# Kernel tuning notes

Measured on AMD Instinct MI355X. Metric: run time of the kernel, lower is better.

Reference implementation:

```python
import jax, jax.numpy as jnp
import numpy as np

B, N, EPG = 64, 512, 8192
E = B * EPG
K1 = int(np.ceil(0.8 * N))    # 410
K2 = int(np.ceil(0.8 * K1))   # 328


def setup_inputs() -> dict:
    key = jax.random.key(0)
    ks = jax.random.split(key, 32)
    x = jax.random.normal(ks[0], (B * N, 32), jnp.float32)
    edge_attr = jax.random.normal(ks[1], (E, 100), jnp.float32)
    src_l = jax.random.randint(ks[2], (E,), 0, N)
    dst_l = jax.random.randint(ks[3], (E,), 0, N)
    off = jnp.repeat(jnp.arange(B, dtype=jnp.int64) * N, EPG)
    edge_index = jnp.stack([src_l + off, dst_l + off]).astype(jnp.int64)
    batch = jnp.repeat(jnp.arange(B, dtype=jnp.int64), N)

    def lin(k, fin, fout):
        s = 1.0 / np.sqrt(fin)
        k1, k2 = jax.random.split(k)
        return (jax.random.uniform(k1, (fin, fout), jnp.float32, -s, s),
                jax.random.uniform(k2, (fout,), jnp.float32, -s, s))

    dec1_w, dec1_b = lin(ks[4], 100, 64)
    dec2_w, dec2_b = lin(ks[5], 64, 32)
    mlp1_w, mlp1_b = lin(ks[6], 32, 128)
    mlp2_w, mlp2_b = lin(ks[7], 128, 256)
    pool1_w = jax.random.normal(ks[8], (256,), jnp.float32) * 0.1
    gat_w = jax.random.normal(ks[9], (256, 256), jnp.float32) * (1.0 / np.sqrt(256))
    gat_att_src = jax.random.normal(ks[10], (4, 64), jnp.float32) * 0.1
    gat_att_dst = jax.random.normal(ks[11], (4, 64), jnp.float32) * 0.1
    gat_b = jnp.zeros((256,), jnp.float32)
    pool2_w = jax.random.normal(ks[12], (256,), jnp.float32) * 0.1
    lin1_w, lin1_b = lin(ks[13], 512, 128)
    lin2_w, lin2_b = lin(ks[14], 128, 64)
    lin3_w, lin3_b = lin(ks[15], 64, 2)
    return dict(x=x, edge_index=edge_index, batch=batch, edge_attr=edge_attr,
                dec1_w=dec1_w, dec1_b=dec1_b, dec2_w=dec2_w, dec2_b=dec2_b,
                mlp1_w=mlp1_w, mlp1_b=mlp1_b, mlp2_w=mlp2_w, mlp2_b=mlp2_b,
                pool1_w=pool1_w, gat_w=gat_w, gat_att_src=gat_att_src,
                gat_att_dst=gat_att_dst, gat_b=gat_b, pool2_w=pool2_w,
                lin1_w=lin1_w, lin1_b=lin1_b, lin2_w=lin2_w, lin2_b=lin2_b,
                lin3_w=lin3_w, lin3_b=lin3_b)


def _forward(x, edge_attr, dec1_w, dec1_b, dec2_w, dec2_b, mlp1_w, mlp1_b,
             mlp2_w, mlp2_b, pool1_w, gat_w, gat_att_src, gat_att_dst, gat_b,
             pool2_w, lin1_w, lin1_b, lin2_w, lin2_b, lin3_w, lin3_b,
             src, dst):
    # edge encoder
    ea = jax.nn.relu(edge_attr @ dec1_w + dec1_b)
    ea = jax.nn.relu(ea @ dec2_w + dec2_b)                       # [E,32]
    # GINEConv (eps=0): sum_j relu(x_j + e_ji), then mlp((1+eps)x + aggr)
    msg = jax.nn.relu(x[src] + ea)
    agg = jax.ops.segment_sum(msg, dst, num_segments=B * N)
    h = x + agg
    h = jax.nn.relu(h @ mlp1_w + mlp1_b) @ mlp2_w + mlp2_b       # [BN,256]
    h = jax.nn.relu(h)
    # TopKPooling 1 (uniform graphs -> fixed k)
    s = jnp.tanh((h @ pool1_w) / jnp.linalg.norm(pool1_w))       # [BN]
    topv, topi = jax.lax.top_k(s.reshape(B, N), K1)              # [B,K1]
    gperm = (topi + jnp.arange(B)[:, None] * N).reshape(-1)
    hp = h[gperm] * topv.reshape(-1)[:, None]                    # [B*K1,256]
    kept = jnp.zeros(B * N, bool).at[gperm].set(True)
    newid = jnp.zeros(B * N, jnp.int32).at[gperm].set(jnp.arange(B * K1, dtype=jnp.int32))
    src1, dst1 = newid[src], newid[dst]
    valid = kept[src] & kept[dst]
    # readout 1: global max + mean pool
    hr = hp.reshape(B, K1, 256)
    x1 = jnp.concatenate([hr.max(axis=1), hr.mean(axis=1)], axis=-1)  # [B,512]
    # GATConv(256, 64, heads=4) with self-loops; invalid edges masked
    Nk = B * K1
    loops = jnp.arange(Nk, dtype=jnp.int32)
    src2 = jnp.concatenate([src1, loops])
    dst2 = jnp.concatenate([dst1, loops])
    valid2 = jnp.concatenate([valid, jnp.ones(Nk, bool)])
    xl = (hp @ gat_w).reshape(Nk, 4, 64)
    a_src = (xl * gat_att_src).sum(-1)                           # [Nk,4]
    a_dst = (xl * gat_att_dst).sum(-1)
    logit = jax.nn.leaky_relu(a_src[src2] + a_dst[dst2], 0.2)    # [E2,4]
    logit = jnp.where(valid2[:, None], logit, -jnp.inf)
    m = jax.ops.segment_max(logit, dst2, num_segments=Nk)
    e = jnp.where(valid2[:, None], jnp.exp(logit - m[dst2]), 0.0)
    den = jax.ops.segment_sum(e, dst2, num_segments=Nk)
    alpha = e / den[dst2]
    out = jax.ops.segment_sum(alpha[:, :, None] * xl[src2], dst2, num_segments=Nk)
    g = jax.nn.relu(out.reshape(Nk, 256) + gat_b)
    # TopKPooling 2 (pooled edges unused downstream)
    s2 = jnp.tanh((g @ pool2_w) / jnp.linalg.norm(pool2_w))
    topv2, topi2 = jax.lax.top_k(s2.reshape(B, K1), K2)
    gperm2 = (topi2 + jnp.arange(B)[:, None] * K1).reshape(-1)
    gp = (g[gperm2] * topv2.reshape(-1)[:, None]).reshape(B, K2, 256)
    x2 = jnp.concatenate([gp.max(axis=1), gp.mean(axis=1)], axis=-1)
    # head (dropout = identity in eval)
    z = x1 + x2
    z = jax.nn.relu(z @ lin1_w + lin1_b)
    z = jax.nn.relu(z @ lin2_w + lin2_b)
    return jax.nn.log_softmax(z @ lin3_w + lin3_b, axis=-1)     # [B,2]


def reference(x, edge_index, batch, edge_attr, dec1_w, dec1_b, dec2_w, dec2_b,
              mlp1_w, mlp1_b, mlp2_w, mlp2_b, pool1_w, gat_w, gat_att_src,
              gat_att_dst, gat_b, pool2_w, lin1_w, lin1_b, lin2_w, lin2_b,
              lin3_w, lin3_b):
    src = edge_index[0].astype(jnp.int32)
    dst = edge_index[1].astype(jnp.int32)
    return _forward(x, edge_attr, dec1_w, dec1_b, dec2_w, dec2_b, mlp1_w,
                    mlp1_b, mlp2_w, mlp2_b, pool1_w, gat_w, gat_att_src,
                    gat_att_dst, gat_b, pool2_w, lin1_w, lin1_b, lin2_w,
                    lin2_b, lin3_w, lin3_b, src, dst)
```

## Files before the change

### kernel.cpp

```cpp
#include <hip/hip_runtime.h>
#include <math.h>

#define B_   64
#define N_   512
#define E_   524288
#define BN_  32768
#define K1_  410
#define K2_  328
#define NK_  26240
#define KC_  25

__device__ __forceinline__ float lrelu(float x) { return x > 0.f ? x : 0.2f * x; }

__global__ __launch_bounds__(256) void norm_kernel(const float* __restrict__ p1,
                                                   const float* __restrict__ p2,
                                                   float* __restrict__ norms) {
    __shared__ float r1[256], r2[256];
    int t = threadIdx.x;
    float a = p1[t], b = p2[t];
    r1[t] = a * a; r2[t] = b * b;
    for (int o = 128; o > 0; o >>= 1) {
        __syncthreads();
        if (t < o) { r1[t] += r1[t + o]; r2[t] += r2[t + o]; }
    }
    __syncthreads();
    if (t == 0) { norms[0] = sqrtf(r1[0]); norms[1] = sqrtf(r2[0]); }
}

template <int NSEG>
__global__ __launch_bounds__(1024) void scan_kernel(int* __restrict__ cnt, int* __restrict__ offsets)
{
    __shared__ int part[1024];
    int t = threadIdx.x;
    const int CH = (NSEG + 1023) / 1024;
    int base = t * CH;
    int sum = 0;
    for (int i = 0; i < CH; ++i) { int gi = base + i; if (gi < NSEG) sum += cnt[gi]; }
    part[t] = sum;
    __syncthreads();
    for (int o = 1; o < 1024; o <<= 1) {
        int v = (t >= o) ? part[t - o] : 0;
        __syncthreads();
        part[t] += v;
        __syncthreads();
    }
    int run = (t == 0) ? 0 : part[t - 1];
    for (int i = 0; i < CH; ++i) {
        int gi = base + i;
        if (gi < NSEG) { offsets[gi] = run; run += cnt[gi]; cnt[gi] = 0; }
    }
    if (t == 1023) offsets[NSEG] = part[1023];
}

__global__ __launch_bounds__(256) void count_node_kernel(const int* __restrict__ dstG,
                                                         int* __restrict__ cnt_node)
{
    int e = blockIdx.x * blockDim.x + threadIdx.x;
    atomicAdd(&cnt_node[dstG[e]], 1);
}

__global__ __launch_bounds__(256) void fill_node_kernel(const int* __restrict__ dstG,
                                                        const int* __restrict__ offs_node,
                                                        int* __restrict__ cnt_node,
                                                        int* __restrict__ pos_e)
{
    int e = blockIdx.x * blockDim.x + threadIdx.x;
    int d = dstG[e];
    int p = offs_node[d] + atomicAdd(&cnt_node[d], 1);
    pos_e[e] = p;
}

__global__ __launch_bounds__(256) void edge_mlp_kernel(
    const float* __restrict__ edge_attr, const int* __restrict__ srcG,
    const int* __restrict__ pos_e,
    const float* __restrict__ x,
    const float* __restrict__ W1, const float* __restrict__ b1,
    const float* __restrict__ W2, const float* __restrict__ b2,
    float* __restrict__ msg_sorted)
{
    __shared__ float bufAT[KC_][68];
    __shared__ float w1cT[KC_][64];
    __shared__ float ea1T[64][68];
    __shared__ float w2s[64][32];
    __shared__ float b2s[32];
    __shared__ int   srcs[64], poss[64];

    int tid = threadIdx.x;
    int eb  = blockIdx.x * 64;

    if (tid < 64) { srcs[tid] = srcG[eb + tid]; poss[tid] = pos_e[eb + tid]; }
    for (int i = tid; i < 64 * 32; i += 256) w2s[i >> 5][i & 31] = W2[i];
    if (tid >= 192 && tid < 224) b2s[tid - 192] = b2[tid - 192];

    int tx = tid & 15, ty = tid >> 4;
    float b1v[4];
#pragma unroll
    for (int j = 0; j < 4; ++j) b1v[j] = b1[tx * 4 + j];

    int attr_base[7], lds_a[7];
    bool valid[7];
#pragma unroll
    for (int u = 0; u < 7; ++u) {
        int i = tid + u * 256;
        valid[u] = (i < 1600);
        int e = i / 25, k = i - e * 25;
        attr_base[u] = (eb + e) * 100 + k;
        lds_a[u] = k * 68 + e;
    }
    float* bufA0 = &bufAT[0][0];
    float* w1l   = &w1cT[0][0];

    float acc[4][4] = {};

    float raA[7], raB[7], rw[7];
    auto issueA = [&](int kc, float (&ra)[7]) {
#pragma unroll
        for (int u = 0; u < 7; ++u)
            if (valid[u]) ra[u] = edge_attr[(size_t)(attr_base[u] + kc)];
    };
    auto issueW = [&](int kc) {
#pragma unroll
        for (int u = 0; u < 7; ++u) {
            int i = tid + u * 256;
            if (valid[u]) rw[u] = W1[(size_t)kc * 64 + i];
        }
    };
    auto lwriteA = [&](float (&ra)[7]) {
#pragma unroll
        for (int u = 0; u < 7; ++u)
            if (valid[u]) bufA0[lds_a[u]] = ra[u];
    };
    auto lwriteW = [&]() {
#pragma unroll
        for (int u = 0; u < 7; ++u) {
            int i = tid + u * 256;
            if (valid[u]) w1l[i] = rw[u];
        }
    };

    issueA(0, raA);
    issueW(0);
    issueA(KC_, raB);
    lwriteA(raA); lwriteW();
    __syncthreads();

#pragma unroll
    for (int c = 0; c < 4; ++c) {
        if (c == 0) issueA(2 * KC_, raA);
        if (c == 1) issueA(3 * KC_, raB);
        if (c < 3)  issueW((c + 1) * KC_);
#pragma unroll 5
        for (int k = 0; k < KC_; ++k) {
            float4 a4 = *(const float4*)&bufAT[k][ty * 4];
            float4 w4 = *(const float4*)&w1cT[k][tx * 4];
            float a[4] = { a4.x, a4.y, a4.z, a4.w };
            float w[4] = { w4.x, w4.y, w4.z, w4.w };
#pragma unroll
            for (int i = 0; i < 4; ++i)
#pragma unroll
                for (int j = 0; j < 4; ++j) acc[i][j] += a[i] * w[j];
        }
        if (c < 3) {
            __syncthreads();
            if ((c & 1) == 0) lwriteA(raB);
            else              lwriteA(raA);
            lwriteW();
            __syncthreads();
        }
    }
#pragma unroll
    for (int j = 0; j < 4; ++j) {
        float4 v;
        v.x = fmaxf(acc[0][j] + b1v[j], 0.f);
        v.y = fmaxf(acc[1][j] + b1v[j], 0.f);
        v.z = fmaxf(acc[2][j] + b1v[j], 0.f);
        v.w = fmaxf(acc[3][j] + b1v[j], 0.f);
        *(float4*)&ea1T[tx * 4 + j][ty * 4] = v;
    }
    __syncthreads();

    int e0 = (tid >> 3) * 2;
    int c0 = (tid & 7) * 4;
    float acc2[2][4] = {};
    for (int k = 0; k < 64; ++k) {
        float2 a2 = *(const float2*)&ea1T[k][e0];
        float4 w4 = *(const float4*)&w2s[k][c0];
        float w[4] = { w4.x, w4.y, w4.z, w4.w };
#pragma unroll
        for (int j = 0; j < 4; ++j) {
            acc2[0][j] += a2.x * w[j]; acc2[1][j] += a2.y * w[j];
        }
    }
#pragma unroll
    for (int r = 0; r < 2; ++r) {
        int e = e0 + r, s = srcs[e];
        const float4 xv = *(const float4*)(x + (size_t)s * 32 + c0);
        float xa[4] = { xv.x, xv.y, xv.z, xv.w };
        float4 m;
        m.x = fmaxf(xa[0] + fmaxf(acc2[r][0] + b2s[c0 + 0], 0.f), 0.f);
        m.y = fmaxf(xa[1] + fmaxf(acc2[r][1] + b2s[c0 + 1], 0.f), 0.f);
        m.z = fmaxf(xa[2] + fmaxf(acc2[r][2] + b2s[c0 + 2], 0.f), 0.f);
        m.w = fmaxf(xa[3] + fmaxf(acc2[r][3] + b2s[c0 + 3], 0.f), 0.f);
        *(float4*)(msg_sorted + (size_t)poss[e] * 32 + c0) = m;
    }
}

__global__ __launch_bounds__(256) void segsum_kernel(const float* __restrict__ msg_sorted,
                                                     const int* __restrict__ offs_n,
                                                     float* __restrict__ agg)
{
    int wid  = (blockIdx.x * blockDim.x + threadIdx.x) >> 6;
    int lane = threadIdx.x & 63;
    if (wid >= BN_) return;
    int off0 = offs_n[wid], off1 = offs_n[wid + 1];
    int col = lane & 31, rr = lane >> 5;
    float sum = 0.f;
    for (int j = off0 + rr; j < off1; j += 2)
        sum += msg_sorted[(size_t)j * 32 + col];
    sum += __shfl_xor(sum, 32);
    if (lane < 32) agg[(size_t)wid * 32 + col] = sum;
}

template <int ACT, bool HASBIAS, bool HASA2, bool GATHER, bool SCORES, bool ATTC>
__global__ __launch_bounds__(256) void gemm_tile128(
    const float* __restrict__ A, const float* __restrict__ A2,
    const int* __restrict__ rowidx, const float* __restrict__ rowscale,
    const float* __restrict__ W, const float* __restrict__ bias,
    float* __restrict__ C, int M, int N, int K,
    const float* __restrict__ pvec, float* __restrict__ pout,
    const float* __restrict__ av_src, const float* __restrict__ av_dst,
    float* __restrict__ ao_src, float* __restrict__ ao_dst)
{
    __shared__ float As[16][132];
    __shared__ float Ws[16][132];
    int tid = threadIdx.x;
    int tx = tid & 15, ty = tid >> 4;
    int mb = blockIdx.y * 128, nb = blockIdx.x * 128;
    float acc[8][8] = {};

    int am = tid & 127;
    int ak = (tid >> 7) * 8;
    int wk = tid >> 4;
    int wn = (tid & 15) * 8;

    int   arow  = mb + am;
    float ascal = 1.f;
    if (GATHER) { ascal = rowscale[arow]; arow = rowidx[arow]; }

    for (int kt = 0; kt < K; kt += 16) {
        {
            const float* pa = A + (size_t)arow * K + kt + ak;
            float4 v0 = *(const float4*)(pa);
            float4 v1 = *(const float4*)(pa + 4);
            if (HASA2) {
                const float* pb = A2 + (size_t)arow * K + kt + ak;
                float4 u0 = *(const float4*)(pb);
                float4 u1 = *(const float4*)(pb + 4);
                v0.x += u0.x; v0.y += u0.y; v0.z += u0.z; v0.w += u0.w;
                v1.x += u1.x; v1.y += u1.y; v1.z += u1.z; v1.w += u1.w;
            }
            if (GATHER) {
                v0.x *= ascal; v0.y *= ascal; v0.z *= ascal; v0.w *= ascal;
                v1.x *= ascal; v1.y *= ascal; v1.z *= ascal; v1.w *= ascal;
            }
            As[ak + 0][am] = v0.x; As[ak + 1][am] = v0.y;
            As[ak + 2][am] = v0.z; As[ak + 3][am] = v0.w;
            As[ak + 4][am] = v1.x; As[ak + 5][am] = v1.y;
            As[ak + 6][am] = v1.z; As[ak + 7][am] = v1.w;
        }
        {
            const float* pw = W + (size_t)(kt + wk) * N + nb + wn;
            *(float4*)&Ws[wk][wn]     = *(const float4*)(pw);
            *(float4*)&Ws[wk][wn + 4] = *(const float4*)(pw + 4);
        }
        __syncthreads();
#pragma unroll
        for (int k2 = 0; k2 < 16; ++k2) {
            float4 a0 = *(const float4*)&As[k2][ty * 8];
            float4 a1 = *(const float4*)&As[k2][ty * 8 + 4];
            float4 w0 = *(const float4*)&Ws[k2][tx * 4];
            float4 w1 = *(const float4*)&Ws[k2][64 + tx * 4];
            float a[8] = { a0.x, a0.y, a0.z, a0.w, a1.x, a1.y, a1.z, a1.w };
            float w[8] = { w0.x, w0.y, w0.z, w0.w, w1.x, w1.y, w1.z, w1.w };
#pragma unroll
            for (int i = 0; i < 8; ++i)
#pragma unroll
                for (int j = 0; j < 8; ++j) acc[i][j] += a[i] * w[j];
        }
        __syncthreads();
    }
    int col0 = nb + tx * 4, col1 = nb + 64 + tx * 4;
    int hd0 = col0 >> 6, hd1 = col1 >> 6;
#pragma unroll
    for (int i = 0; i < 8; ++i) {
        int m = mb + ty * 8 + i;
        float r[8];
#pragma unroll
        for (int j = 0; j < 4; ++j) {
            float v = acc[i][j];
            if (HASBIAS) v += bias[col0 + j];
            if (ACT == 1) v = fmaxf(v, 0.f);
            r[j] = v;
        }
#pragma unroll
        for (int j = 4; j < 8; ++j) {
            float v = acc[i][j];
            if (HASBIAS) v += bias[col1 + j - 4];
            if (ACT == 1) v = fmaxf(v, 0.f);
            r[j] = v;
        }
        float4 o0 = { r[0], r[1], r[2], r[3] };
        float4 o1 = { r[4], r[5], r[6], r[7] };
        *(float4*)&C[(size_t)m * N + col0] = o0;
        *(float4*)&C[(size_t)m * N + col1] = o1;

        if (SCORES) {
            float d = 0.f;
#pragma unroll
            for (int j = 0; j < 4; ++j) d += r[j] * pvec[col0 + j];
#pragma unroll
            for (int j = 4; j < 8; ++j) d += r[j] * pvec[col1 + j - 4];
#pragma unroll
            for (int o = 1; o < 16; o <<= 1) d += __shfl_xor(d, o);
            if (tx == 0) atomicAdd(&pout[m], d);
        }
        if (ATTC) {
            float sA = 0.f, sB = 0.f, dA = 0.f, dB = 0.f;
#pragma unroll
            for (int j = 0; j < 4; ++j) {
                int w0i = hd0 * 64 + ((col0 & 63) + j);
                int w1i = hd1 * 64 + ((col1 & 63) + j);
                sA += r[j] * av_src[w0i];   dA += r[j] * av_dst[w0i];
                sB += r[j + 4] * av_src[w1i]; dB += r[j + 4] * av_dst[w1i];
            }
#pragma unroll
            for (int o = 1; o < 16; o <<= 1) {
                sA += __shfl_xor(sA, o); sB += __shfl_xor(sB, o);
                dA += __shfl_xor(dA, o); dB += __shfl_xor(dB, o);
            }
            if (tx == 0) {
                atomicAdd(&ao_src[m * 4 + hd0], sA);
                atomicAdd(&ao_src[m * 4 + hd1], sB);
                atomicAdd(&ao_dst[m * 4 + hd0], dA);
                atomicAdd(&ao_dst[m * 4 + hd1], dB);
            }
        }
    }
}

__global__ __launch_bounds__(256) void scores_fin_kernel(float* __restrict__ s,
                                                         const float* __restrict__ norms,
                                                         int R)
{
    int i = blockIdx.x * blockDim.x + threadIdx.x;
    if (i < R) s[i] = tanhf(s[i] / norms[0]);
}

__device__ void bitonic_desc512(float* val, int* idx, int t) {
    for (int k = 2; k <= 512; k <<= 1) {
        for (int j = k >> 1; j > 0; j >>= 1) {
            __syncthreads();
            int ixj = t ^ j;
            if (ixj > t) {
                float v0 = val[t], v1 = val[ixj];
                int   i0 = idx[t], i1 = idx[ixj];
                bool before = (v0 > v1) || (v0 == v1 && i0 < i1);
                bool dir = ((t & k) == 0);
                bool doswap = dir ? (!before) : before;
                if (doswap) { val[t] = v1; val[ixj] = v0; idx[t] = i1; idx[ixj] = i0; }
            }
        }
    }
    __syncthreads();
}

__global__ __launch_bounds__(512) void topk1_kernel(const float* __restrict__ s,
                                                    float* __restrict__ topval,
                                                    int* __restrict__ topnode,
                                                    int* __restrict__ kept,
                                                    int* __restrict__ newid)
{
    __shared__ float val[512];
    __shared__ int   idx[512];
    int b = blockIdx.x, t = threadIdx.x;
    val[t] = s[b * N_ + t]; idx[t] = t;
    bitonic_desc512(val, idx, t);
    if (t < K1_) {
        int node = b * N_ + idx[t];
        int orow = b * K1_ + t;
        topnode[orow] = node;
        topval[orow]  = val[t];
        kept[node]  = 1;
        newid[node] = orow;
    }
}

__global__ __launch_bounds__(1024) void readout1_kernel(const float* __restrict__ h,
                                                        const int* __restrict__ topnode,
                                                        const float* __restrict__ topval,
                                                        float* __restrict__ zbuf)
{
    __shared__ float rmx[1024], rsm[1024];
    int b = blockIdx.x >> 2, cg = blockIdx.x & 3;
    int tid = threadIdx.x;
    int cl = tid & 63, rg = tid >> 6;
    int c = cg * 64 + cl;
    float mx = -INFINITY, sm = 0.f;
    for (int j = rg; j < K1_; j += 16) {
        int row = topnode[b * K1_ + j];
        float v = h[(size_t)row * 256 + c] * topval[b * K1_ + j];
        mx = fmaxf(mx, v); sm += v;
    }
    rmx[tid] = mx; rsm[tid] = sm;
    __syncthreads();
    if (tid < 512) { rmx[tid] = fmaxf(rmx[tid], rmx[tid + 512]); rsm[tid] += rsm[tid + 512]; }
    __syncthreads();
    if (tid < 256) { rmx[tid] = fmaxf(rmx[tid], rmx[tid + 256]); rsm[tid] += rsm[tid + 256]; }
    __syncthreads();
    if (tid < 128) { rmx[tid] = fmaxf(rmx[tid], rmx[tid + 128]); rsm[tid] += rsm[tid + 128]; }
    __syncthreads();
    if (tid < 64) {
        zbuf[b * 512 + c]       = fmaxf(rmx[tid], rmx[tid + 64]);
        zbuf[b * 512 + 256 + c] = (rsm[tid] + rsm[tid + 64]) / (float)K1_;
    }
}

__global__ __launch_bounds__(256) void count_kernel(const int* __restrict__ srcG,
                                                    const int* __restrict__ dstG,
                                                    const int* __restrict__ kept,
                                                    const int* __restrict__ newid,
                                                    int* __restrict__ cnt)
{
    int e = blockIdx.x * blockDim.x + threadIdx.x;
    int s = srcG[e], d = dstG[e];
    if (kept[s] && kept[d]) atomicAdd(&cnt[newid[d]], 1);
}

__global__ __launch_bounds__(256) void fill_kernel(const int* __restrict__ srcG,
                                                   const int* __restrict__ dstG,
                                                   const int* __restrict__ kept,
                                                   const int* __restrict__ newid,
                                                   const int* __restrict__ offsets,
                                                   int* __restrict__ cnt,
                                                   int* __restrict__ csr_src)
{
    int e = blockIdx.x * blockDim.x + threadIdx.x;
    int s = srcG[e], d = dstG[e];
    if (kept[s] && kept[d]) {
        int d1 = newid[d];
        int p = offsets[d1] + atomicAdd(&cnt[d1], 1);
        csr_src[p] = newid[s];
    }
}

__global__ __launch_bounds__(256) void gat_agg_kernel(const float* __restrict__ xl,
                                                      const float* __restrict__ a_src,
                                                      const float* __restrict__ a_dst,
                                                      const int* __restrict__ offsets,
                                                      const int* __restrict__ csr_src,
                                                      const float* __restrict__ gat_b,
                                                      const float* __restrict__ pool2_w,
                                                      const float* __restrict__ norms,
                                                      float* __restrict__ g,
                                                      float* __restrict__ s2)
{
    int wid  = (blockIdx.x * blockDim.x + threadIdx.x) >> 6;
    int lane = threadIdx.x & 63;
    if (wid >= NK_) return;
    int off0 = offsets[wid], off1 = offsets[wid + 1];

    float4 ad = *(const float4*)(a_dst + (size_t)wid * 4);
    float4 asf = *(const float4*)(a_src + (size_t)wid * 4);
    float adv[4] = { ad.x, ad.y, ad.z, ad.w };
    float lsf[4] = { lrelu(asf.x + ad.x), lrelu(asf.y + ad.y),
                     lrelu(asf.z + ad.z), lrelu(asf.w + ad.w) };

    float den[4] = {};
    float acc[4] = {};
    int e = off0;
    for (; e + 1 < off1; e += 2) {
        int s1 = csr_src[e], s2v = csr_src[e + 1];
        float4 a1 = *(const float4*)(a_src + (size_t)s1 * 4);
        float4 a2 = *(const float4*)(a_src + (size_t)s2v * 4);
        float av1[4] = { a1.x, a1.y, a1.z, a1.w };
        float av2[4] = { a2.x, a2.y, a2.z, a2.w };
#pragma unroll
        for (int r = 0; r < 4; ++r) {
            float w1 = expf(fminf(lrelu(av1[r] + adv[r]), 80.f));
            float w2 = expf(fminf(lrelu(av2[r] + adv[r]), 80.f));
            float x1 = xl[(size_t)s1 * 256 + r * 64 + lane];
            float x2 = xl[(size_t)s2v * 256 + r * 64 + lane];
            den[r] += w1 + w2;
            acc[r] += w1 * x1 + w2 * x2;
        }
    }
    if (e < off1) {
        int s1 = csr_src[e];
        float4 a1 = *(const float4*)(a_src + (size_t)s1 * 4);
        float av1[4] = { a1.x, a1.y, a1.z, a1.w };
#pragma unroll
        for (int r = 0; r < 4; ++r) {
            float w1 = expf(fminf(lrelu(av1[r] + adv[r]), 80.f));
            den[r] += w1;
            acc[r] += w1 * xl[(size_t)s1 * 256 + r * 64 + lane];
        }
    }
    float gv[4];
#pragma unroll
    for (int r = 0; r < 4; ++r) {
        float ws = expf(fminf(lsf[r], 80.f));
        den[r] += ws;
        acc[r] = (acc[r] + ws * xl[(size_t)wid * 256 + r * 64 + lane]) / den[r];
        int d = r * 64 + lane;
        gv[r] = fmaxf(acc[r] + gat_b[d], 0.f);
        g[(size_t)wid * 256 + d] = gv[r];
    }
    float dot = 0.f;
#pragma unroll
    for (int r = 0; r < 4; ++r) dot += gv[r] * pool2_w[r * 64 + lane];
    for (int o = 32; o > 0; o >>= 1) dot += __shfl_xor(dot, o);
    if (lane == 0) s2[wid] = tanhf(dot / norms[1]);
}

__global__ __launch_bounds__(512) void topk2_sort_kernel(const float* __restrict__ s2,
                                                         int* __restrict__ t2row,
                                                         float* __restrict__ t2val)
{
    __shared__ float val[512];
    __shared__ int   idx[512];
    int b = blockIdx.x, t = threadIdx.x;
    val[t] = (t < K1_) ? s2[b * K1_ + t] : -INFINITY;
    idx[t] = t;
    bitonic_desc512(val, idx, t);
    if (t < K2_) {
        t2row[b * K2_ + t] = b * K1_ + idx[t];
        t2val[b * K2_ + t] = val[t];
    }
}

__global__ __launch_bounds__(512) void readout2_kernel(const float* __restrict__ g,
                                                       const int* __restrict__ t2row,
                                                       const float* __restrict__ t2val,
                                                       float* __restrict__ zbuf)
{
    __shared__ float rmx[512], rsm[512];
    int b = blockIdx.x >> 2, cg = blockIdx.x & 3;
    int tid = threadIdx.x;
    int cl = tid & 63, rg = tid >> 6;
    int c = cg * 64 + cl;
    float mx = -INFINITY, sm = 0.f;
    for (int j = rg; j < K2_; j += 8) {
        int row = t2row[b * K2_ + j];
        float v = g[(size_t)row * 256 + c] * t2val[b * K2_ + j];
        mx = fmaxf(mx, v); sm += v;
    }
    rmx[tid] = mx; rsm[tid] = sm;
    __syncthreads();
    if (tid < 256) { rmx[tid] = fmaxf(rmx[tid], rmx[tid + 256]); rsm[tid] += rsm[tid + 256]; }
    __syncthreads();
    if (tid < 128) { rmx[tid] = fmaxf(rmx[tid], rmx[tid + 128]); rsm[tid] += rsm[tid + 128]; }
    __syncthreads();
    if (tid < 64) {
        zbuf[b * 512 + c]       += fmaxf(rmx[tid], rmx[tid + 64]);
        zbuf[b * 512 + 256 + c] += (rsm[tid] + rsm[tid + 64]) / (float)K2_;
    }
}

__global__ __launch_bounds__(128) void head_kernel(const float* __restrict__ zbuf,
                                                   const float* __restrict__ l1w, const float* __restrict__ l1b,
                                                   const float* __restrict__ l2w, const float* __restrict__ l2b,
                                                   const float* __restrict__ l3w, const float* __restrict__ l3b,
                                                   float* __restrict__ out)
{
    __shared__ float zs[512];
    __shared__ float h1s[128];
    __shared__ float h2s[64];
    __shared__ float os[2];
    int b = blockIdx.x, t = threadIdx.x;
    for (int i = t; i < 512; i += 128) zs[i] = zbuf[b * 512 + i];
    __syncthreads();
    float acc = l1b[t];
    for (int k = 0; k < 512; ++k) acc += zs[k] * l1w[k * 128 + t];
    h1s[t] = fmaxf(acc, 0.f);
    __syncthreads();
    if (t < 64) {
        float a2 = l2b[t];
        for (int k = 0; k < 128; ++k) a2 += h1s[k] * l2w[k * 64 + t];
        h2s[t] = fmaxf(a2, 0.f);
    }
    __syncthreads();
    if (t < 2) {
        float a3 = l3b[t];
        for (int k = 0; k < 64; ++k) a3 += h2s[k] * l3w[k * 2 + t];
        os[t] = a3;
    }
    __syncthreads();
    if (t == 0) {
        float m = fmaxf(os[0], os[1]);
        float lse = m + logf(expf(os[0] - m) + expf(os[1] - m));
        out[b * 2 + 0] = os[0] - lse;
        out[b * 2 + 1] = os[1] - lse;
    }
}

extern "C" void kernel_launch(void* const* d_in, const int* in_sizes, int n_in,
                              void* d_out, int out_size, void* d_ws, size_t ws_size,
                              hipStream_t stream)
{
    const float* x         = (const float*)d_in[0];
    const int*   eidx      = (const int*)d_in[1];
    const float* edge_attr = (const float*)d_in[3];
    const float* dec1_w    = (const float*)d_in[4];
    const float* dec1_b    = (const float*)d_in[5];
    const float* dec2_w    = (const float*)d_in[6];
    const float* dec2_b    = (const float*)d_in[7];
    const float* mlp1_w    = (const float*)d_in[8];
    const float* mlp1_b    = (const float*)d_in[9];
    const float* mlp2_w    = (const float*)d_in[10];
    const float* mlp2_b    = (const float*)d_in[11];
    const float* pool1_w   = (const float*)d_in[12];
    const float* gat_w     = (const float*)d_in[13];
    const float* att_src   = (const float*)d_in[14];
    const float* att_dst   = (const float*)d_in[15];
    const float* gat_b     = (const float*)d_in[16];
    const float* pool2_w   = (const float*)d_in[17];
    const float* lin1_w    = (const float*)d_in[18];
    const float* lin1_b    = (const float*)d_in[19];
    const float* lin2_w    = (const float*)d_in[20];
    const float* lin2_b    = (const float*)d_in[21];
    const float* lin3_w    = (const float*)d_in[22];
    const float* lin3_b    = (const float*)d_in[23];
    const int* srcG = eidx;
    const int* dstG = eidx + E_;
    float* out = (float*)d_out;

    char* base = (char*)d_ws;
    size_t o = 0;
    auto alloc = [&](size_t bytes) { size_t r = o; o = (o + bytes + 255) & ~(size_t)255; return r; };
    size_t agg_off    = alloc((size_t)BN_ * 32 * 4);
    size_t cntn_off   = alloc((size_t)BN_ * 4);
    size_t cnt_off    = alloc((size_t)NK_ * 4);
    size_t kept_off   = alloc((size_t)BN_ * 4);
    size_t s_off      = alloc((size_t)BN_ * 4);
    size_t asrc_off   = alloc((size_t)NK_ * 4 * 4);
    size_t adst_off   = alloc((size_t)NK_ * 4 * 4);
    size_t zero_bytes = o;
    size_t newid_off  = alloc((size_t)BN_ * 4);
    size_t offsn_off  = alloc((size_t)(BN_ + 1) * 4);
    size_t pos_off    = alloc((size_t)E_ * 4);
    size_t h_off      = alloc((size_t)BN_ * 256 * 4);
    size_t hp_off     = alloc((size_t)NK_ * 256 * 4);
    size_t xl_off     = alloc((size_t)NK_ * 256 * 4);
    size_t tnode_off  = alloc((size_t)NK_ * 4);
    size_t tval_off   = alloc((size_t)NK_ * 4);
    size_t offs_off   = alloc((size_t)(NK_ + 1) * 4);
    size_t csr_off    = alloc((size_t)E_ * 4);
    size_t zbuf_off   = alloc((size_t)B_ * 512 * 4);
    size_t norm_off   = alloc(256);
    if (o > ws_size) return;

    float* agg      = (float*)(base + agg_off);
    int*   cnt_node = (int*)  (base + cntn_off);
    int*   cnt      = (int*)  (base + cnt_off);
    int*   kept     = (int*)  (base + kept_off);
    float* s        = (float*)(base + s_off);
    float* a_src    = (float*)(base + asrc_off);
    float* a_dst    = (float*)(base + adst_off);
    int*   newid    = (int*)  (base + newid_off);
    int*   offs_n   = (int*)  (base + offsn_off);
    int*   pos_e    = (int*)  (base + pos_off);
    float* h        = (float*)(base + h_off);
    float* g        = h;
    float* msg      = h;
    float* xl       = (float*)(base + xl_off);
    float* t1       = xl;
    int*   tnode    = (int*)  (base + tnode_off);
    float* tval     = (float*)(base + tval_off);
    int*   offs     = (int*)  (base + offs_off);
    int*   csr      = (int*)  (base + csr_off);
    float* zbuf     = (float*)(base + zbuf_off);
    float* norms    = (float*)(base + norm_off);

    hipMemsetAsync(d_ws, 0, zero_bytes, stream);

    norm_kernel<<<1, 256, 0, stream>>>(pool1_w, pool2_w, norms);

    count_node_kernel<<<E_ / 256, 256, 0, stream>>>(dstG, cnt_node);
    scan_kernel<BN_><<<1, 1024, 0, stream>>>(cnt_node, offs_n);
    fill_node_kernel<<<E_ / 256, 256, 0, stream>>>(dstG, offs_n, cnt_node, pos_e);

    edge_mlp_kernel<<<E_ / 64, 256, 0, stream>>>(edge_attr, srcG, pos_e, x,
                                                 dec1_w, dec1_b, dec2_w, dec2_b, msg);
    segsum_kernel<<<BN_ / 4, 256, 0, stream>>>(msg, offs_n, agg);

    gemm_tile128<1, true, true, false, false, false><<<dim3(1, BN_ / 128), 256, 0, stream>>>(
        x, agg, nullptr, nullptr, mlp1_w, mlp1_b, t1, BN_, 128, 32,
        nullptr, nullptr, nullptr, nullptr, nullptr, nullptr);
    gemm_tile128<1, true, false, false, true, false><<<dim3(2, BN_ / 128), 256, 0, stream>>>(
        t1, nullptr, nullptr, nullptr, mlp2_w, mlp2_b, h, BN_, 256, 128,
        pool1_w, s, nullptr, nullptr, nullptr, nullptr);

    scores_fin_kernel<<<BN_ / 256, 256, 0, stream>>>(s, norms, BN_);
    topk1_kernel<<<B_, 512, 0, stream>>>(s, tval, tnode, kept, newid);
    readout1_kernel<<<B_ * 4, 1024, 0, stream>>>(h, tnode, tval, zbuf);

    gemm_tile128<0, false, false, true, false, true><<<dim3(2, NK_ / 128), 256, 0, stream>>>(
        h, nullptr, tnode, tval, gat_w, nullptr, xl, NK_, 256, 256,
        nullptr, nullptr, att_src, att_dst, a_src, a_dst);

    count_kernel<<<E_ / 256, 256, 0, stream>>>(srcG, dstG, kept, newid, cnt);
    scan_kernel<NK_><<<1, 1024, 0, stream>>>(cnt, offs);
    fill_kernel<<<E_ / 256, 256, 0, stream>>>(srcG, dstG, kept, newid, offs, cnt, csr);

    gat_agg_kernel<<<NK_ / 4, 256, 0, stream>>>(xl, a_src, a_dst, offs, csr, gat_b,
                                                pool2_w, norms, g, s);

    topk2_sort_kernel<<<B_, 512, 0, stream>>>(s, tnode, tval);
    readout2_kernel<<<B_ * 4, 512, 0, stream>>>(g, tnode, tval, zbuf);

    head_kernel<<<B_, 128, 0, stream>>>(zbuf, lin1_w, lin1_b, lin2_w, lin2_b,
                                        lin3_w, lin3_b, out);
}
```

Before: 552.9 us.

## Reuse first-stage dst CSR for GAT aggregation, drop second CSR build

The destination-sorted edge permutation from the first stage is kept and reused by the GAT aggregation, which filters edges on the fly with kept/newid. The separate count, scan and fill kernels that built a compacted CSR for pooled nodes go away. The tanh score finalisation is folded into the top-k kernels, relying on tanh being monotonic, so only selected values are transformed. In exchange, gat_agg now does extra indirect loads (csr_e, srcG, kept) for edges that are later discarded, loses its two-edge unrolled loop, and the agg buffer is moved out of the memset region.

```diff
diff --git a/kernel.cpp b/kernel.cpp
--- a/kernel.cpp
+++ b/kernel.cpp
@@ -62,12 +62,14 @@
 __global__ __launch_bounds__(256) void fill_node_kernel(const int* __restrict__ dstG,
                                                         const int* __restrict__ offs_node,
                                                         int* __restrict__ cnt_node,
-                                                        int* __restrict__ pos_e)
+                                                        int* __restrict__ pos_e,
+                                                        int* __restrict__ csr_e)
 {
     int e = blockIdx.x * blockDim.x + threadIdx.x;
     int d = dstG[e];
     int p = offs_node[d] + atomicAdd(&cnt_node[d], 1);
     pos_e[e] = p;
+    csr_e[p] = e;
 }
 
 __global__ __launch_bounds__(256) void edge_mlp_kernel(
@@ -348,14 +350,6 @@
     }
 }
 
-__global__ __launch_bounds__(256) void scores_fin_kernel(float* __restrict__ s,
-                                                         const float* __restrict__ norms,
-                                                         int R)
-{
-    int i = blockIdx.x * blockDim.x + threadIdx.x;
-    if (i < R) s[i] = tanhf(s[i] / norms[0]);
-}
-
 __device__ void bitonic_desc512(float* val, int* idx, int t) {
     for (int k = 2; k <= 512; k <<= 1) {
         for (int j = k >> 1; j > 0; j >>= 1) {
@@ -375,6 +369,7 @@
 }
 
 __global__ __launch_bounds__(512) void topk1_kernel(const float* __restrict__ s,
+                                                    const float* __restrict__ norms,
                                                     float* __restrict__ topval,
                                                     int* __restrict__ topnode,
                                                     int* __restrict__ kept,
@@ -389,7 +384,7 @@
         int node = b * N_ + idx[t];
         int orow = b * K1_ + t;
         topnode[orow] = node;
-        topval[orow]  = val[t];
+        topval[orow]  = tanhf(val[t] / norms[0]);
         kept[node]  = 1;
         newid[node] = orow;
     }
@@ -425,49 +420,25 @@
     }
 }
 
-__global__ __launch_bounds__(256) void count_kernel(const int* __restrict__ srcG,
-                                                    const int* __restrict__ dstG,
-                                                    const int* __restrict__ kept,
-                                                    const int* __restrict__ newid,
-                                                    int* __restrict__ cnt)
-{
-    int e = blockIdx.x * blockDim.x + threadIdx.x;
-    int s = srcG[e], d = dstG[e];
-    if (kept[s] && kept[d]) atomicAdd(&cnt[newid[d]], 1);
-}
-
-__global__ __launch_bounds__(256) void fill_kernel(const int* __restrict__ srcG,
-                                                   const int* __restrict__ dstG,
-                                                   const int* __restrict__ kept,
-                                                   const int* __restrict__ newid,
-                                                   const int* __restrict__ offsets,
-                                                   int* __restrict__ cnt,
-                                                   int* __restrict__ csr_src)
-{
-    int e = blockIdx.x * blockDim.x + threadIdx.x;
-    int s = srcG[e], d = dstG[e];
-    if (kept[s] && kept[d]) {
-        int d1 = newid[d];
-        int p = offsets[d1] + atomicAdd(&cnt[d1], 1);
-        csr_src[p] = newid[s];
-    }
-}
-
 __global__ __launch_bounds__(256) void gat_agg_kernel(const float* __restrict__ xl,
                                                       const float* __restrict__ a_src,
                                                       const float* __restrict__ a_dst,
-                                                      const int* __restrict__ offsets,
-                                                      const int* __restrict__ csr_src,
+                                                      const int* __restrict__ tnode,
+                                                      const int* __restrict__ offs_n,
+                                                      const int* __restrict__ csr_e,
+                                                      const int* __restrict__ srcG,
+                                                      const int* __restrict__ kept,
+                                                      const int* __restrict__ newid,
                                                       const float* __restrict__ gat_b,
                                                       const float* __restrict__ pool2_w,
-                                                      const float* __restrict__ norms,
                                                       float* __restrict__ g,
                                                       float* __restrict__ s2)
 {
     int wid  = (blockIdx.x * blockDim.x + threadIdx.x) >> 6;
     int lane = threadIdx.x & 63;
     if (wid >= NK_) return;
-    int off0 = offsets[wid], off1 = offsets[wid + 1];
+    int orig = tnode[wid];
+    int off0 = offs_n[orig], off1 = offs_n[orig + 1];
 
     float4 ad = *(const float4*)(a_dst + (size_t)wid * 4);
     float4 asf = *(const float4*)(a_src + (size_t)wid * 4);
@@ -477,25 +448,11 @@
 
     float den[4] = {};
     float acc[4] = {};
-    int e = off0;
-    for (; e + 1 < off1; e += 2) {
-        int s1 = csr_src[e], s2v = csr_src[e + 1];
-        float4 a1 = *(const float4*)(a_src + (size_t)s1 * 4);
-        float4 a2 = *(const float4*)(a_src + (size_t)s2v * 4);
-        float av1[4] = { a1.x, a1.y, a1.z, a1.w };
-        float av2[4] = { a2.x, a2.y, a2.z, a2.w };
-#pragma unroll
-        for (int r = 0; r < 4; ++r) {
-            float w1 = expf(fminf(lrelu(av1[r] + adv[r]), 80.f));
-            float w2 = expf(fminf(lrelu(av2[r] + adv[r]), 80.f));
-            float x1 = xl[(size_t)s1 * 256 + r * 64 + lane];
-            float x2 = xl[(size_t)s2v * 256 + r * 64 + lane];
-            den[r] += w1 + w2;
-            acc[r] += w1 * x1 + w2 * x2;
-        }
-    }
-    if (e < off1) {
-        int s1 = csr_src[e];
+    for (int p = off0; p < off1; ++p) {
+        int e = csr_e[p];
+        int srcn = srcG[e];
+        if (!kept[srcn]) continue;
+        int s1 = newid[srcn];
         float4 a1 = *(const float4*)(a_src + (size_t)s1 * 4);
         float av1[4] = { a1.x, a1.y, a1.z, a1.w };
 #pragma unroll
@@ -519,10 +476,11 @@
 #pragma unroll
     for (int r = 0; r < 4; ++r) dot += gv[r] * pool2_w[r * 64 + lane];
     for (int o = 32; o > 0; o >>= 1) dot += __shfl_xor(dot, o);
-    if (lane == 0) s2[wid] = tanhf(dot / norms[1]);
+    if (lane == 0) s2[wid] = dot;
 }
 
 __global__ __launch_bounds__(512) void topk2_sort_kernel(const float* __restrict__ s2,
+                                                         const float* __restrict__ norms,
                                                          int* __restrict__ t2row,
                                                          float* __restrict__ t2val)
 {
@@ -534,7 +492,7 @@
     bitonic_desc512(val, idx, t);
     if (t < K2_) {
         t2row[b * K2_ + t] = b * K1_ + idx[t];
-        t2val[b * K2_ + t] = val[t];
+        t2val[b * K2_ + t] = tanhf(val[t] / norms[1]);
     }
 }
 
@@ -637,38 +595,36 @@
     char* base = (char*)d_ws;
     size_t o = 0;
     auto alloc = [&](size_t bytes) { size_t r = o; o = (o + bytes + 255) & ~(size_t)255; return r; };
-    size_t agg_off    = alloc((size_t)BN_ * 32 * 4);
     size_t cntn_off   = alloc((size_t)BN_ * 4);
-    size_t cnt_off    = alloc((size_t)NK_ * 4);
     size_t kept_off   = alloc((size_t)BN_ * 4);
     size_t s_off      = alloc((size_t)BN_ * 4);
     size_t asrc_off   = alloc((size_t)NK_ * 4 * 4);
     size_t adst_off   = alloc((size_t)NK_ * 4 * 4);
     size_t zero_bytes = o;
+    size_t agg_off    = alloc((size_t)BN_ * 32 * 4);
     size_t newid_off  = alloc((size_t)BN_ * 4);
     size_t offsn_off  = alloc((size_t)(BN_ + 1) * 4);
     size_t pos_off    = alloc((size_t)E_ * 4);
+    size_t csre_off   = alloc((size_t)E_ * 4);
     size_t h_off      = alloc((size_t)BN_ * 256 * 4);
     size_t hp_off     = alloc((size_t)NK_ * 256 * 4);
     size_t xl_off     = alloc((size_t)NK_ * 256 * 4);
     size_t tnode_off  = alloc((size_t)NK_ * 4);
     size_t tval_off   = alloc((size_t)NK_ * 4);
-    size_t offs_off   = alloc((size_t)(NK_ + 1) * 4);
-    size_t csr_off    = alloc((size_t)E_ * 4);
     size_t zbuf_off   = alloc((size_t)B_ * 512 * 4);
     size_t norm_off   = alloc(256);
     if (o > ws_size) return;
 
-    float* agg      = (float*)(base + agg_off);
     int*   cnt_node = (int*)  (base + cntn_off);
-    int*   cnt      = (int*)  (base + cnt_off);
     int*   kept     = (int*)  (base + kept_off);
     float* s        = (float*)(base + s_off);
     float* a_src    = (float*)(base + asrc_off);
     float* a_dst    = (float*)(base + adst_off);
+    float* agg      = (float*)(base + agg_off);
     int*   newid    = (int*)  (base + newid_off);
     int*   offs_n   = (int*)  (base + offsn_off);
     int*   pos_e    = (int*)  (base + pos_off);
+    int*   csr_e    = (int*)  (base + csre_off);
     float* h        = (float*)(base + h_off);
     float* g        = h;
     float* msg      = h;
@@ -676,8 +632,6 @@
     float* t1       = xl;
     int*   tnode    = (int*)  (base + tnode_off);
     float* tval     = (float*)(base + tval_off);
-    int*   offs     = (int*)  (base + offs_off);
-    int*   csr      = (int*)  (base + csr_off);
     float* zbuf     = (float*)(base + zbuf_off);
     float* norms    = (float*)(base + norm_off);
 
@@ -687,7 +641,7 @@
 
     count_node_kernel<<<E_ / 256, 256, 0, stream>>>(dstG, cnt_node);
     scan_kernel<BN_><<<1, 1024, 0, stream>>>(cnt_node, offs_n);
-    fill_node_kernel<<<E_ / 256, 256, 0, stream>>>(dstG, offs_n, cnt_node, pos_e);
+    fill_node_kernel<<<E_ / 256, 256, 0, stream>>>(dstG, offs_n, cnt_node, pos_e, csr_e);
 
     edge_mlp_kernel<<<E_ / 64, 256, 0, stream>>>(edge_attr, srcG, pos_e, x,
                                                  dec1_w, dec1_b, dec2_w, dec2_b, msg);
@@ -700,22 +654,17 @@
         t1, nullptr, nullptr, nullptr, mlp2_w, mlp2_b, h, BN_, 256, 128,
         pool1_w, s, nullptr, nullptr, nullptr, nullptr);
 
-    scores_fin_kernel<<<BN_ / 256, 256, 0, stream>>>(s, norms, BN_);
-    topk1_kernel<<<B_, 512, 0, stream>>>(s, tval, tnode, kept, newid);
+    topk1_kernel<<<B_, 512, 0, stream>>>(s, norms, tval, tnode, kept, newid);
     readout1_kernel<<<B_ * 4, 1024, 0, stream>>>(h, tnode, tval, zbuf);
 
     gemm_tile128<0, false, false, true, false, true><<<dim3(2, NK_ / 128), 256, 0, stream>>>(
         h, nullptr, tnode, tval, gat_w, nullptr, xl, NK_, 256, 256,
         nullptr, nullptr, att_src, att_dst, a_src, a_dst);
 
-    count_kernel<<<E_ / 256, 256, 0, stream>>>(srcG, dstG, kept, newid, cnt);
-    scan_kernel<NK_><<<1, 1024, 0, stream>>>(cnt, offs);
-    fill_kernel<<<E_ / 256, 256, 0, stream>>>(srcG, dstG, kept, newid, offs, cnt, csr);
-
-    gat_agg_kernel<<<NK_ / 4, 256, 0, stream>>>(xl, a_src, a_dst, offs, csr, gat_b,
-                                                pool2_w, norms, g, s);
-
-    topk2_sort_kernel<<<B_, 512, 0, stream>>>(s, tnode, tval);
+    gat_agg_kernel<<<NK_ / 4, 256, 0, stream>>>(xl, a_src, a_dst, tnode, offs_n, csr_e,
+                                                srcG, kept, newid, gat_b, pool2_w, g, s);
+
+    topk2_sort_kernel<<<B_, 512, 0, stream>>>(s, norms, tnode, tval);
     readout2_kernel<<<B_ * 4, 512, 0, stream>>>(g, tnode, tval, zbuf);
 
     head_kernel<<<B_, 128, 0, stream>>>(zbuf, lin1_w, lin1_b, lin2_w, lin2_b,
```

Measured after the change: 527.6 us. -4.6%, faster.
